# Optimization experiments

Hardware: AMD Instinct MI355X
Metric: run time of the kernel (lower is better)

Reference implementation:

```python
import jax, jax.numpy as jnp
import numpy as np

N = 100000      # nodes
DEG = 16        # fixed degree
E = N * DEG     # edges
C_IN = 128
C_OUT = 128


def setup_inputs() -> dict:
    key = jax.random.key(0)
    k1, k2, k3, k4, k5 = jax.random.split(key, 5)
    x = jax.random.normal(k1, (N, C_IN), dtype=jnp.float32)
    # glorot-ish init for the dense weight
    scale = jnp.sqrt(6.0 / (C_IN + C_OUT)).astype(jnp.float32)
    weight = jax.random.uniform(k2, (C_IN, C_OUT), dtype=jnp.float32, minval=-1.0, maxval=1.0) * scale
    bias = jax.random.normal(k3, (C_OUT,), dtype=jnp.float32) * 0.02
    # fixed-degree CSR: every node has DEG in-edges; CSC analogously
    rowptr = (jnp.arange(N + 1, dtype=jnp.int32) * DEG)
    colind = jax.random.randint(k4, (E,), 0, N, dtype=jnp.int32)
    colptr = (jnp.arange(N + 1, dtype=jnp.int32) * DEG)
    rowind = jax.random.randint(k5, (E,), 0, N, dtype=jnp.int32)
    return {"x": x, "weight": weight, "bias": bias,
            "rowptr": rowptr, "colind": colind,
            "colptr": colptr, "rowind": rowind}


def _deg_inv_sqrt(indptr, dtype):
    deg = (indptr[1:] - indptr[:-1]).astype(dtype)
    return (1.0 / jnp.sqrt(deg))[:, None]  # [N, 1]


def reference(x, weight, bias, rowptr, colind, colptr, rowind):
    # dense transform: [N, C_in] @ [C_in, C_out]
    h = x @ weight
    in_norm = _deg_inv_sqrt(rowptr, h.dtype)    # 1/sqrt(in-degree)
    out_norm = _deg_inv_sqrt(colptr, h.dtype)   # 1/sqrt(out-degree)
    h = h * out_norm
    # CSR SpMM (unweighted): out[i] = sum_{e in [rowptr[i], rowptr[i+1])} h[colind[e]]
    n_nodes = rowptr.shape[0] - 1
    n_edges = colind.shape[0]
    row = jnp.searchsorted(rowptr, jnp.arange(n_edges, dtype=rowptr.dtype), side="right") - 1
    aggr = jax.ops.segment_sum(h[colind], row, num_segments=n_nodes)
    aggr = aggr * in_norm + bias
    return aggr
```

## Files before the change

kernel.cpp:

```cpp
#include <hip/hip_runtime.h>
#include <hip/hip_bf16.h>

#define N_NODES 100000
#define DEG 16
#define C 128
#define NTILES 6250
#define FBLOCKS 2048
#define PREPBLKS 6250
#define WQBLKS 8

typedef __attribute__((ext_vector_type(8))) short short8;
typedef __attribute__((ext_vector_type(4))) float f32x4;

__device__ inline unsigned short f2bf(float f) {
    unsigned int u = __builtin_bit_cast(unsigned int, f);
    u += 0x7fffu + ((u >> 16) & 1u);
    return (unsigned short)(u >> 16);
}

__global__ __launch_bounds__(256, 8)
void gcn_prep_kernel(const float* __restrict__ x, const float* __restrict__ wmat,
                     unsigned char* __restrict__ x8, float* __restrict__ scale,
                     unsigned short* __restrict__ wq)
{
    int tid = threadIdx.x;

    if (blockIdx.x >= PREPBLKS) {
        int s  = (blockIdx.x - PREPBLKS) * 256 + tid;
        int nt = s >> 8;
        int kc = (s >> 6) & 3;
        int ln = s & 63;
        int g  = ln >> 4;
        int cl = ln & 15;
        short8 w;
#pragma unroll
        for (int j = 0; j < 8; ++j)
            w[j] = (short)f2bf(wmat[(kc * 32 + g * 8 + j) * C + nt * 16 + cl]);
        *reinterpret_cast<short8*>(wq + (size_t)s * 8) = w;
        return;
    }

    int wave = tid >> 6;
    int lane = tid & 63;
    int row = (blockIdx.x * 4 + wave) * 4 + (lane >> 4);
    int cg = lane & 15;

    const float* xr = x + (long)row * C + cg * 8;
    f32x4 a = *reinterpret_cast<const f32x4*>(xr);
    f32x4 b = *reinterpret_cast<const f32x4*>(xr + 4);

    float m = fmaxf(fmaxf(fmaxf(fabsf(a[0]), fabsf(a[1])), fmaxf(fabsf(a[2]), fabsf(a[3]))),
                    fmaxf(fmaxf(fabsf(b[0]), fabsf(b[1])), fmaxf(fabsf(b[2]), fabsf(b[3]))));
    m = fmaxf(m, __shfl_xor(m, 1));
    m = fmaxf(m, __shfl_xor(m, 2));
    m = fmaxf(m, __shfl_xor(m, 4));
    m = fmaxf(m, __shfl_xor(m, 8));
    m = fmaxf(m, 1e-30f);

    float inv = 127.0f / m;
    unsigned int lo = 0, hi = 0;
    lo |= ((unsigned int)((int)rintf(a[0] * inv) + 128));
    lo |= ((unsigned int)((int)rintf(a[1] * inv) + 128)) << 8;
    lo |= ((unsigned int)((int)rintf(a[2] * inv) + 128)) << 16;
    lo |= ((unsigned int)((int)rintf(a[3] * inv) + 128)) << 24;
    hi |= ((unsigned int)((int)rintf(b[0] * inv) + 128));
    hi |= ((unsigned int)((int)rintf(b[1] * inv) + 128)) << 8;
    hi |= ((unsigned int)((int)rintf(b[2] * inv) + 128)) << 16;
    hi |= ((unsigned int)((int)rintf(b[3] * inv) + 128)) << 24;

    uint2 pk; pk.x = lo; pk.y = hi;
    *reinterpret_cast<uint2*>(x8 + (long)row * C + cg * 8) = pk;

    if (cg == 0) {
        scale[row] = m * (0.0625f / 127.0f);
    }
}

__device__ __forceinline__ uint4 dq_pack(const uint2* v, float mysc, int gb, float fix)
{
    float acc[8] = {0.f, 0.f, 0.f, 0.f, 0.f, 0.f, 0.f, 0.f};
#pragma unroll
    for (int e = 0; e < 16; ++e) {
        float s = __shfl(mysc, gb + e);
        unsigned int a = v[e].x, b = v[e].y;
        acc[0] += s * (float)(a & 0xff);
        acc[1] += s * (float)((a >> 8) & 0xff);
        acc[2] += s * (float)((a >> 16) & 0xff);
        acc[3] += s * (float)(a >> 24);
        acc[4] += s * (float)(b & 0xff);
        acc[5] += s * (float)((b >> 8) & 0xff);
        acc[6] += s * (float)((b >> 16) & 0xff);
        acc[7] += s * (float)(b >> 24);
    }
    uint4 o;
    o.x = (unsigned int)f2bf(acc[0] - fix) |
          ((unsigned int)f2bf(acc[1] - fix) << 16);
    o.y = (unsigned int)f2bf(acc[2] - fix) |
          ((unsigned int)f2bf(acc[3] - fix) << 16);
    o.z = (unsigned int)f2bf(acc[4] - fix) |
          ((unsigned int)f2bf(acc[5] - fix) << 16);
    o.w = (unsigned int)f2bf(acc[6] - fix) |
          ((unsigned int)f2bf(acc[7] - fix) << 16);
    return o;
}

__device__ __forceinline__ float subgroup_sum16(float s)
{
    s += __shfl_xor(s, 1);
    s += __shfl_xor(s, 2);
    s += __shfl_xor(s, 4);
    s += __shfl_xor(s, 8);
    return s;
}

__global__ __launch_bounds__(256, 4)
void gcn_fused_kernel(const unsigned char* __restrict__ x8,
                      const float* __restrict__ scale,
                      const int* __restrict__ colind,
                      const unsigned short* __restrict__ wq,
                      const float* __restrict__ bias,
                      float* __restrict__ out)
{
    __shared__ uint4 atile[2][16 * 16];

    int tid  = threadIdx.x;
    int wv   = tid >> 6;
    int lane = tid & 63;
    int g    = lane >> 4;
    int cl   = lane & 15;
    int gb   = lane & 48;
    int r    = wv * 4 + g;

    int t = blockIdx.x;

    int idx0 = colind[t * 256 + r * 16 + cl];

    short8 bw[2][4];
    float  bv[2];
#pragma unroll
    for (int n = 0; n < 2; ++n) {
        int nt = wv * 2 + n;
#pragma unroll
        for (int kc = 0; kc < 4; ++kc)
            bw[n][kc] = *reinterpret_cast<const short8*>(
                wq + (size_t)((nt * 4 + kc) * 64 + lane) * 8);
        bv[n] = bias[nt * 16 + cl];
    }

    float sc0 = scale[idx0];

    {
        uint2 v[16];
#pragma unroll
        for (int e = 0; e < 16; ++e) {
            int j = __shfl(idx0, gb + e);
            v[e] = *reinterpret_cast<const uint2*>(x8 + (j << 7) + (cl << 3));
        }
        int t1 = t + FBLOCKS;
        int idxn = 0; float scn = 0.f;
        if (t1 < NTILES) {
            idxn = colind[t1 * 256 + r * 16 + cl];
            scn  = scale[idxn];
        }
        float fix0 = 128.0f * subgroup_sum16(sc0);
        atile[0][r * 16 + (cl ^ (r & 7))] = dq_pack(v, sc0, gb, fix0);
        __syncthreads();

        int p = 0;
        while (true) {
            int tn = t + FBLOCKS;
            bool more = tn < NTILES;

            uint2 nv[16];
            float sc_c = scn;
            if (more) {
#pragma unroll
                for (int e = 0; e < 16; ++e) {
                    int j = __shfl(idxn, gb + e);
                    nv[e] = *reinterpret_cast<const uint2*>(x8 + (j << 7) + (cl << 3));
                }
                int t2 = tn + FBLOCKS;
                if (t2 < NTILES) {
                    idxn = colind[t2 * 256 + r * 16 + cl];
                    scn  = scale[idxn];
                }
            }

            short8 af[4];
#pragma unroll
            for (int kc = 0; kc < 4; ++kc)
                af[kc] = __builtin_bit_cast(short8,
                    atile[p][cl * 16 + ((kc * 4 + g) ^ (cl & 7))]);

#pragma unroll
            for (int n = 0; n < 2; ++n) {
                f32x4 acc = {0.f, 0.f, 0.f, 0.f};
#pragma unroll
                for (int kc = 0; kc < 4; ++kc)
                    acc = __builtin_amdgcn_mfma_f32_16x16x32_bf16(af[kc], bw[n][kc], acc, 0, 0, 0);
                float* op = out + (long)(t * 16 + g * 4) * C + (wv * 2 + n) * 16 + cl;
#pragma unroll
                for (int r2 = 0; r2 < 4; ++r2)
                    op[r2 * C] = acc[r2] + bv[n];
            }

            if (!more) break;

            float fixn = 128.0f * subgroup_sum16(sc_c);
            atile[p ^ 1][r * 16 + (cl ^ (r & 7))] = dq_pack(nv, sc_c, gb, fixn);
            __syncthreads();
            t = tn;
            p ^= 1;
        }
    }
}

extern "C" void kernel_launch(void* const* d_in, const int* in_sizes, int n_in,
                              void* d_out, int out_size, void* d_ws, size_t ws_size,
                              hipStream_t stream) {
    const float* x      = (const float*)d_in[0];
    const float* w      = (const float*)d_in[1];
    const float* bias   = (const float*)d_in[2];
    const int*   colind = (const int*)d_in[4];
    float* out = (float*)d_out;

    unsigned char*  x8    = (unsigned char*)d_ws;
    float*          scale = (float*)((char*)d_ws + (size_t)N_NODES * C);
    unsigned short* wq    = (unsigned short*)((char*)d_ws + (size_t)N_NODES * C
                                              + (size_t)N_NODES * sizeof(float));

    gcn_prep_kernel<<<PREPBLKS + WQBLKS, 256, 0, stream>>>(x, w, x8, scale, wq);
    gcn_fused_kernel<<<FBLOCKS, 256, 0, stream>>>(x8, scale, colind, wq, bias, out);
}
```

Before: 145.4 us.

## Give each wave a full 16-node tile with bf16 weights staged in LDS

The fused kernel now makes each wave independently own a 16-node tile. Each wave gathers and dequantizes the neighbour rows in four K-chunks directly into MFMA A-fragments and multiplies them against the whole 128x128 bf16 weight matrix, which is staged once per block in 32KB of LDS. This removes the per-tile LDS round trip for the aggregated tile and the block-wide __syncthreads, and software-pipelines the next chunk's gathers and next tile's index loads. In exchange it uses more registers (8 accumulators, double-buffered gathers), lowers launch bounds to 3 and halves the block count. It also reads weights from LDS on every tile.

```diff
diff --git a/kernel.cpp b/kernel.cpp
--- a/kernel.cpp
+++ b/kernel.cpp
@@ -5,7 +5,7 @@
 #define DEG 16
 #define C 128
 #define NTILES 6250
-#define FBLOCKS 2048
+#define FBLOCKS 1024
 #define PREPBLKS 6250
 #define WQBLKS 8
 
@@ -76,44 +76,7 @@
     }
 }
 
-__device__ __forceinline__ uint4 dq_pack(const uint2* v, float mysc, int gb, float fix)
-{
-    float acc[8] = {0.f, 0.f, 0.f, 0.f, 0.f, 0.f, 0.f, 0.f};
-#pragma unroll
-    for (int e = 0; e < 16; ++e) {
-        float s = __shfl(mysc, gb + e);
-        unsigned int a = v[e].x, b = v[e].y;
-        acc[0] += s * (float)(a & 0xff);
-        acc[1] += s * (float)((a >> 8) & 0xff);
-        acc[2] += s * (float)((a >> 16) & 0xff);
-        acc[3] += s * (float)(a >> 24);
-        acc[4] += s * (float)(b & 0xff);
-        acc[5] += s * (float)((b >> 8) & 0xff);
-        acc[6] += s * (float)((b >> 16) & 0xff);
-        acc[7] += s * (float)(b >> 24);
-    }
-    uint4 o;
-    o.x = (unsigned int)f2bf(acc[0] - fix) |
-          ((unsigned int)f2bf(acc[1] - fix) << 16);
-    o.y = (unsigned int)f2bf(acc[2] - fix) |
-          ((unsigned int)f2bf(acc[3] - fix) << 16);
-    o.z = (unsigned int)f2bf(acc[4] - fix) |
-          ((unsigned int)f2bf(acc[5] - fix) << 16);
-    o.w = (unsigned int)f2bf(acc[6] - fix) |
-          ((unsigned int)f2bf(acc[7] - fix) << 16);
-    return o;
-}
-
-__device__ __forceinline__ float subgroup_sum16(float s)
-{
-    s += __shfl_xor(s, 1);
-    s += __shfl_xor(s, 2);
-    s += __shfl_xor(s, 4);
-    s += __shfl_xor(s, 8);
-    return s;
-}
-
-__global__ __launch_bounds__(256, 4)
+__global__ __launch_bounds__(256, 3)
 void gcn_fused_kernel(const unsigned char* __restrict__ x8,
                       const float* __restrict__ scale,
                       const int* __restrict__ colind,
@@ -121,97 +84,120 @@
                       const float* __restrict__ bias,
                       float* __restrict__ out)
 {
-    __shared__ uint4 atile[2][16 * 16];
-
-    int tid  = threadIdx.x;
-    int wv   = tid >> 6;
+    __shared__ uint4 wlds[2048];
+
+    int tid = threadIdx.x;
+#pragma unroll
+    for (int i = 0; i < 8; ++i)
+        wlds[i * 256 + tid] =
+            *reinterpret_cast<const uint4*>(wq + (size_t)(i * 256 + tid) * 8);
+
     int lane = tid & 63;
-    int g    = lane >> 4;
-    int cl   = lane & 15;
-    int gb   = lane & 48;
-    int r    = wv * 4 + g;
-
-    int t = blockIdx.x;
-
-    int idx0 = colind[t * 256 + r * 16 + cl];
-
-    short8 bw[2][4];
-    float  bv[2];
-#pragma unroll
-    for (int n = 0; n < 2; ++n) {
-        int nt = wv * 2 + n;
-#pragma unroll
-        for (int kc = 0; kc < 4; ++kc)
-            bw[n][kc] = *reinterpret_cast<const short8*>(
-                wq + (size_t)((nt * 4 + kc) * 64 + lane) * 8);
-        bv[n] = bias[nt * 16 + cl];
-    }
-
-    float sc0 = scale[idx0];
-
-    {
-        uint2 v[16];
+    int m    = lane & 15;
+    int o    = lane >> 4;
+
+    float bv[8];
+#pragma unroll
+    for (int nt = 0; nt < 8; ++nt) bv[nt] = bias[nt * 16 + m];
+
+    __syncthreads();
+
+    const int nwaves = FBLOCKS * 4;
+    int t = blockIdx.x * 4 + (tid >> 6);
+    if (t >= NTILES) return;
+
+    int   idxq[4];
+    float scq[4];
+#pragma unroll
+    for (int q = 0; q < 4; ++q)
+        idxq[q] = colind[t * 256 + m * 16 + o * 4 + q];
+#pragma unroll
+    for (int q = 0; q < 4; ++q)
+        scq[q] = scale[idxq[q]];
+
+    while (true) {
+        float fs = (scq[0] + scq[1]) + (scq[2] + scq[3]);
+        fs += __shfl_xor(fs, 16);
+        fs += __shfl_xor(fs, 32);
+        float fix = 128.0f * fs;
+
+        f32x4 acc[8];
+#pragma unroll
+        for (int nt = 0; nt < 8; ++nt) acc[nt] = f32x4{0.f, 0.f, 0.f, 0.f};
+
+        uint2 v[2][16];
 #pragma unroll
         for (int e = 0; e < 16; ++e) {
-            int j = __shfl(idx0, gb + e);
-            v[e] = *reinterpret_cast<const uint2*>(x8 + (j << 7) + (cl << 3));
+            int j = __shfl(idxq[e & 3], ((e >> 2) << 4) + m);
+            v[0][e] = *reinterpret_cast<const uint2*>(
+                x8 + ((long)j << 7) + o * 8);
         }
-        int t1 = t + FBLOCKS;
-        int idxn = 0; float scn = 0.f;
-        if (t1 < NTILES) {
-            idxn = colind[t1 * 256 + r * 16 + cl];
-            scn  = scale[idxn];
+
+        int  tn   = t + nwaves;
+        bool more = tn < NTILES;
+        int   idxq2[4];
+        float scq2[4];
+
+#pragma unroll
+        for (int kc = 0; kc < 4; ++kc) {
+            if (kc < 3) {
+#pragma unroll
+                for (int e = 0; e < 16; ++e) {
+                    int j = __shfl(idxq[e & 3], ((e >> 2) << 4) + m);
+                    v[(kc + 1) & 1][e] = *reinterpret_cast<const uint2*>(
+                        x8 + ((long)j << 7) + (kc + 1) * 32 + o * 8);
+                }
+            }
+            if (kc == 0 && more) {
+#pragma unroll
+                for (int q = 0; q < 4; ++q)
+                    idxq2[q] = colind[tn * 256 + m * 16 + o * 4 + q];
+            }
+            if (kc == 2 && more) {
+#pragma unroll
+                for (int q = 0; q < 4; ++q)
+                    scq2[q] = scale[idxq2[q]];
+            }
+
+            float da[8] = {0.f, 0.f, 0.f, 0.f, 0.f, 0.f, 0.f, 0.f};
+#pragma unroll
+            for (int e = 0; e < 16; ++e) {
+                float s = __shfl(scq[e & 3], ((e >> 2) << 4) + m);
+                unsigned int a = v[kc & 1][e].x, b = v[kc & 1][e].y;
+                da[0] += s * (float)(a & 0xff);
+                da[1] += s * (float)((a >> 8) & 0xff);
+                da[2] += s * (float)((a >> 16) & 0xff);
+                da[3] += s * (float)(a >> 24);
+                da[4] += s * (float)(b & 0xff);
+                da[5] += s * (float)((b >> 8) & 0xff);
+                da[6] += s * (float)((b >> 16) & 0xff);
+                da[7] += s * (float)(b >> 24);
+            }
+            short8 af;
+#pragma unroll
+            for (int i = 0; i < 8; ++i)
+                af[i] = (short)f2bf(da[i] - fix);
+
+#pragma unroll
+            for (int nt = 0; nt < 8; ++nt) {
+                short8 wf = __builtin_bit_cast(short8,
+                    wlds[(nt * 4 + kc) * 64 + lane]);
+                acc[nt] = __builtin_amdgcn_mfma_f32_16x16x32_bf16(
+                    af, wf, acc[nt], 0, 0, 0);
+            }
         }
-        float fix0 = 128.0f * subgroup_sum16(sc0);
-        atile[0][r * 16 + (cl ^ (r & 7))] = dq_pack(v, sc0, gb, fix0);
-        __syncthreads();
-
-        int p = 0;
-        while (true) {
-            int tn = t + FBLOCKS;
-            bool more = tn < NTILES;
-
-            uint2 nv[16];
-            float sc_c = scn;
-            if (more) {
-#pragma unroll
-                for (int e = 0; e < 16; ++e) {
-                    int j = __shfl(idxn, gb + e);
-                    nv[e] = *reinterpret_cast<const uint2*>(x8 + (j << 7) + (cl << 3));
-                }
-                int t2 = tn + FBLOCKS;
-                if (t2 < NTILES) {
-                    idxn = colind[t2 * 256 + r * 16 + cl];
-                    scn  = scale[idxn];
-                }
-            }
-
-            short8 af[4];
-#pragma unroll
-            for (int kc = 0; kc < 4; ++kc)
-                af[kc] = __builtin_bit_cast(short8,
-                    atile[p][cl * 16 + ((kc * 4 + g) ^ (cl & 7))]);
-
-#pragma unroll
-            for (int n = 0; n < 2; ++n) {
-                f32x4 acc = {0.f, 0.f, 0.f, 0.f};
-#pragma unroll
-                for (int kc = 0; kc < 4; ++kc)
-                    acc = __builtin_amdgcn_mfma_f32_16x16x32_bf16(af[kc], bw[n][kc], acc, 0, 0, 0);
-                float* op = out + (long)(t * 16 + g * 4) * C + (wv * 2 + n) * 16 + cl;
-#pragma unroll
-                for (int r2 = 0; r2 < 4; ++r2)
-                    op[r2 * C] = acc[r2] + bv[n];
-            }
-
-            if (!more) break;
-
-            float fixn = 128.0f * subgroup_sum16(sc_c);
-            atile[p ^ 1][r * 16 + (cl ^ (r & 7))] = dq_pack(nv, sc_c, gb, fixn);
-            __syncthreads();
-            t = tn;
-            p ^= 1;
-        }
+
+        float* op = out + (long)(t * 16 + o * 4) * C + m;
+#pragma unroll
+        for (int nt = 0; nt < 8; ++nt)
+#pragma unroll
+            for (int r2 = 0; r2 < 4; ++r2)
+                op[(long)r2 * C + nt * 16] = acc[nt][r2] + bv[nt];
+
+        if (!more) break;
+        t = tn;
+#pragma unroll
+        for (int q = 0; q < 4; ++q) { idxq[q] = idxq2[q]; scq[q] = scq2[q]; }
     }
 }
 
```

Result: slower. 234.7 us (+61.4%).
